# Optimization experiments

Hardware: AMD Instinct MI355X
Metric: run time of the kernel (lower is better)

Reference implementation:

```python
import jax, jax.numpy as jnp
import numpy as np

P_SCALAR = 40.0
NEG_INF = -1e9


def setup_inputs() -> dict:
    key = jax.random.key(0)
    ks = jax.random.split(key, 6)
    B, Dk, Dv, T, H, W = 2, 128, 512, 2, 64, 64
    qkey = jax.random.normal(ks[0], (B, Dk, H, W), dtype=jnp.float32)
    qval = jax.random.normal(ks[1], (B, Dv, H, W), dtype=jnp.float32)
    mkey = jax.random.normal(ks[2], (B, Dk, T, H, W), dtype=jnp.float32)
    mval = jax.random.normal(ks[3], (B, Dv, T, H, W), dtype=jnp.float32)
    qmask = jax.random.bernoulli(ks[4], 0.5, (B, 1, H, W))
    mmask = jax.random.bernoulli(ks[5], 0.5, (B, 1, T, H, W))
    return {"qkey": qkey, "qval": qval, "qmask": qmask,
            "mkey": mkey, "mval": mval, "mmask": mmask}


def reference(qkey, qval, qmask, mkey, mval, mmask):
    # Faithful vectorized version of maskRead: for each batch, attention from
    # masked query pixels over masked memory pixels, scatter back into zeros.
    # Boolean-gather + softmax over gathered rows == full softmax with masked
    # logits set to -inf (rows outside mmask get zero probability).
    B, Dk, H, W = qkey.shape
    Dv = qval.shape[1]
    qk = qkey.reshape(B, Dk, H * W)            # [B, Dk, Nq]
    mk = mkey.reshape(B, Dk, -1)               # [B, Dk, Nm]
    mv = mval.reshape(B, Dv, -1)               # [B, Dv, Nm]
    qm = qmask.reshape(B, H * W)               # [B, Nq]
    mm = mmask.reshape(B, -1)                  # [B, Nm]

    # p[b, m, q] = <mk[b,:,m], qk[b,:,q]> * p_scalar, softmax over m
    p = jnp.einsum('bdm,bdq->bmq', mk, qk) * P_SCALAR
    p = jnp.where(mm[:, :, None], p, NEG_INF)
    p = jax.nn.softmax(p, axis=1)              # [B, Nm, Nq]

    read = jnp.einsum('bvm,bmq->bvq', mv, p)   # [B, Dv, Nq]

    # zero out query pixels outside qmask; skip batches with empty masks
    valid = qm[:, None, :] & mm.any(axis=1)[:, None, None] & qm.any(axis=1)[:, None, None]
    qread = jnp.where(valid, read, 0.0)
    return qread.reshape(B, Dv, H, W)
```

## Files before the change

### kernel.cpp

```cpp
#include <hip/hip_runtime.h>

#define NQ 4096
#define NM 8192
#define DK 128
#define DV 512
#define BATCH 2
#define NT (NM / 64)
#define KTS 8192
#define VTILE 16384

typedef __attribute__((ext_vector_type(8))) short short8;
typedef __attribute__((ext_vector_type(4))) float f32x4;
typedef unsigned short ushort_t;

#define MF(A_, B_, C_) __builtin_amdgcn_mfma_f32_16x16x32_bf16(A_, B_, C_, 0, 0, 0)

static __device__ __forceinline__ unsigned short f2bf(float x) {
    union { float f; unsigned int u; } c; c.f = x;
    unsigned int u = c.u;
    return (unsigned short)((u + 0x7FFFu + ((u >> 16) & 1u)) >> 16);
}
static __device__ __forceinline__ float bf2f(unsigned short h) {
    union { unsigned int u; float f; } c; c.u = ((unsigned int)h) << 16;
    return c.f;
}

static __device__ __forceinline__ size_t vaddr(int b, int pos, int dv) {
    const int mt = pos >> 6, m64 = pos & 63;
    const int dvh = dv >> 8, rr = dv & 255;
    return (((size_t)(b * NT + mt) * 2 + dvh) * VTILE)
         + (rr >> 6) * 4096 + ((rr >> 4) & 3) * 1024
         + (m64 >> 5) * 512
         + ((((m64 >> 4) & 1) * 2 + ((m64 >> 3) & 1)) * 128)
         + (rr & 15) * 8 + (m64 & 7);
}

#define LOADK(AH, AL, itn_) do {                                              \
    const size_t ktb_ = kbase + (size_t)(itn_) * KTS;                         \
    _Pragma("unroll")                                                         \
    for (int ks_ = 0; ks_ < 4; ++ks_) {                                       \
        AH[ks_] = *(const short8*)(kh0 + ktb_ + ks_ * 512);                   \
        AL[ks_] = *(const short8*)(kl0 + ktb_ + ks_ * 512);                   \
    }                                                                         \
} while (0)

__global__ __launch_bounds__(1024) void scan_kernel(
    const int* __restrict__ qmask, const int* __restrict__ mmask,
    int* __restrict__ cidx, int* __restrict__ cpos,
    int* __restrict__ cnts, int* __restrict__ qflags) {
    const int b = blockIdx.x;
    const int t = threadIdx.x;
    const int lane = t & 63;
    const int w = t >> 6;
    __shared__ int wsum[16];
    __shared__ int qsh;

    const int* mp = mmask + b * NM;
    const int base = t * 8;
    int val[8];
#pragma unroll
    for (int i = 0; i < 8; ++i) val[i] = (mp[base + i] != 0);
    int c0 = 0;
#pragma unroll
    for (int i = 0; i < 8; ++i) c0 += val[i];

    int c = c0;
#pragma unroll
    for (int off = 1; off < 64; off <<= 1) {
        int n = __shfl_up(c, off, 64);
        if (lane >= off) c += n;
    }
    if (lane == 63) wsum[w] = c;
    if (t == 0) qsh = 0;
    __syncthreads();
    if (t == 0) {
        int s = 0;
#pragma unroll
        for (int i = 0; i < 16; ++i) { s += wsum[i]; wsum[i] = s; }
    }
    __syncthreads();
    const int wbase = (w == 0) ? 0 : wsum[w - 1];
    int run = wbase + (c - c0);
#pragma unroll
    for (int i = 0; i < 8; ++i) {
        int m = base + i;
        cpos[b * NM + m] = run;
        if (val[i]) { cidx[b * NM + run] = m; ++run; }
    }

    int qa = 0;
    for (int i = t; i < NQ; i += 1024) qa |= (qmask[b * NQ + i] != 0);
    if (qa) atomicOr(&qsh, 1);
    __syncthreads();
    if (t == 0) { cnts[b] = wsum[15]; qflags[b] = qsh; }
}

__global__ __launch_bounds__(256) void prep_q_kernel(
    const float* __restrict__ src, ushort_t* __restrict__ hi,
    ushort_t* __restrict__ lo) {
    const int b = blockIdx.z;
    const int d0 = blockIdx.y * 32;
    const int n0 = blockIdx.x * 32;
    __shared__ float t32[32][33];
    for (int l = threadIdx.x; l < 1024; l += 256) {
        int r = l >> 5, c = l & 31;
        t32[r][c] = src[((size_t)b * DK + d0 + r) * NQ + n0 + c];
    }
    __syncthreads();
    for (int l = threadIdx.x; l < 1024; l += 256) {
        int r = l >> 5, c = l & 31;
        float f = t32[c][r];
        unsigned short h = f2bf(f);
        unsigned short lw = f2bf(f - bf2f(h));
        size_t off = ((size_t)b * NQ + n0 + r) * DK + d0 + c;
        hi[off] = h;
        lo[off] = lw;
    }
}

__global__ __launch_bounds__(256) void prep_k_kernel(
    const float* __restrict__ src, const int* __restrict__ mmask,
    const int* __restrict__ cpos,
    ushort_t* __restrict__ hi, ushort_t* __restrict__ lo) {
    const int b = blockIdx.z;
    const int d0 = blockIdx.y * 32;
    const int n0 = blockIdx.x * 32;
    __shared__ float t32[32][33];
    for (int l = threadIdx.x; l < 1024; l += 256) {
        int r = l >> 5, c = l & 31;
        t32[r][c] = src[((size_t)b * DK + d0 + r) * NM + n0 + c];
    }
    __syncthreads();
    for (int l = threadIdx.x; l < 1024; l += 256) {
        int r = l >> 5, c = l & 31;
        int m = n0 + r;
        if (mmask[b * NM + m] != 0) {
            int pos = cpos[b * NM + m];
            float f = t32[c][r];
            unsigned short h = f2bf(f);
            unsigned short lw = f2bf(f - bf2f(h));
            int d = d0 + c;
            size_t off = ((size_t)(b * NT + (pos >> 6))) * KTS
                       + ((pos >> 4) & 3) * 2048 + (d >> 5) * 512
                       + ((d >> 3) & 3) * 128 + (pos & 15) * 8 + (d & 7);
            hi[off] = h;
            lo[off] = lw;
        }
    }
}

__global__ __launch_bounds__(256) void prep_v_kernel(
    const float* __restrict__ src, const int* __restrict__ mmask,
    const int* __restrict__ cpos, const int* __restrict__ cnts,
    ushort_t* __restrict__ dst) {
    const int b = blockIdx.z;
    const int dv0 = blockIdx.x * 8;
    if (blockIdx.y == 8) {
        const int cnt = cnts[b];
        const int pend = ((cnt + 63) >> 6) * 64;
        const int dv = dv0 + (threadIdx.x >> 5);
        for (int p = cnt + (threadIdx.x & 31); p < pend; p += 32)
            dst[vaddr(b, p, dv)] = 0;
        return;
    }
    const int m = blockIdx.y * 1024 + threadIdx.x * 4;
    const int4 mm = *(const int4*)(mmask + b * NM + m);
    const int4 cp = *(const int4*)(cpos + b * NM + m);
#pragma unroll
    for (int i = 0; i < 8; ++i) {
        const int dv = dv0 + i;
        const float4 v = *(const float4*)(src + ((size_t)b * DV + dv) * NM + m);
        if (mm.x) dst[vaddr(b, cp.x, dv)] = f2bf(v.x);
        if (mm.y) dst[vaddr(b, cp.y, dv)] = f2bf(v.y);
        if (mm.z) dst[vaddr(b, cp.z, dv)] = f2bf(v.z);
        if (mm.w) dst[vaddr(b, cp.w, dv)] = f2bf(v.w);
    }
}

__global__ __launch_bounds__(256, 4) void stats_kernel(
    const ushort_t* __restrict__ Qhi, const ushort_t* __restrict__ Khi,
    const int* __restrict__ cnts, float* __restrict__ mpart) {
    const int t = threadIdx.x;
    const int lane = t & 63;
    const int w = t >> 6;
    const int quad = lane >> 4;
    const int col = lane & 15;
    const int bid = blockIdx.x;
    const int part = bid & 3;
    const int b = (bid >> 2) & 1;
    const int qb = (bid >> 3) * 32;

    const int cnt = cnts[b];
    const int nit = (cnt + 63) >> 6;
    const int it0 = (nit * part) >> 2;
    const int it1 = (nit * (part + 1)) >> 2;

    __shared__ float red_m[4][32];

    short8 qfh[2][4];
    {
        const ushort_t* qhp = Qhi + ((size_t)b * NQ + qb) * DK;
#pragma unroll
        for (int qt = 0; qt < 2; ++qt)
#pragma unroll
            for (int ks = 0; ks < 4; ++ks)
                qfh[qt][ks] = *(const short8*)(qhp + (size_t)(qt * 16 + col) * DK + ks * 32 + quad * 8);
    }

    const f32x4 zero4 = {0.f, 0.f, 0.f, 0.f};
    float mloc[2] = {-3.0e38f, -3.0e38f};
    const ushort_t* kh0 = Khi + w * 2048 + lane * 8;
    const size_t kbase = (size_t)(b * NT) * KTS;

#define LOADKH(A_, itn_) do {                                                 \
    const size_t ktb_ = kbase + (size_t)(itn_) * KTS;                         \
    _Pragma("unroll")                                                         \
    for (int ks_ = 0; ks_ < 4; ++ks_)                                         \
        A_[ks_] = *(const short8*)(kh0 + ktb_ + ks_ * 512);                   \
} while (0)

#define STPH(CK, NK, it_, itn_) do {                                          \
    LOADKH(NK, itn_);                                                         \
    f32x4 aS0 = zero4, aS1 = zero4;                                           \
    _Pragma("unroll")                                                         \
    for (int ks = 0; ks < 4; ++ks) {                                          \
        aS0 = MF(CK[ks], qfh[0][ks], aS0);                                    \
        aS1 = MF(CK[ks], qfh[1][ks], aS1);                                    \
    }                                                                         \
    const int mrow_ = (it_) * 64 + w * 16 + quad * 4;                         \
    _Pragma("unroll")                                                         \
    for (int r = 0; r < 4; ++r) {                                             \
        if (mrow_ + r < cnt) {                                                \
            mloc[0] = fmaxf(mloc[0], aS0[r] * 40.0f);                         \
            mloc[1] = fmaxf(mloc[1], aS1[r] * 40.0f);                         \
        }                                                                     \
    }                                                                         \
} while (0)

    short8 kA[4], kB[4];
    int it = it0;
    if (it < it1) {
        LOADKH(kA, it);
        int itn;
        while (true) {
            itn = (it + 1 < it1) ? it + 1 : it;
            STPH(kA, kB, it, itn);
            if (++it >= it1) break;
            itn = (it + 1 < it1) ? it + 1 : it;
            STPH(kB, kA, it, itn);
            if (++it >= it1) break;
        }
    }
#undef STPH
#undef LOADKH

#pragma unroll
    for (int qt = 0; qt < 2; ++qt) {
        float m = mloc[qt];
        m = fmaxf(m, __shfl_xor(m, 16, 64));
        m = fmaxf(m, __shfl_xor(m, 32, 64));
        if (lane < 16) red_m[w][qt * 16 + col] = m;
    }
    __syncthreads();
    if (t < 32) {
        float M = -3.0e38f;
#pragma unroll
        for (int ww = 0; ww < 4; ++ww) M = fmaxf(M, red_m[ww][t]);
        mpart[((size_t)(b * 4 + part)) * NQ + qb + t] = M;
    }
}

__global__ __launch_bounds__(256, 2) void pv_kernel(
    const ushort_t* __restrict__ Qhi, const ushort_t* __restrict__ Qlo,
    const ushort_t* __restrict__ Khi, const ushort_t* __restrict__ Klo,
    const ushort_t* __restrict__ Vimg, const int* __restrict__ cnts,
    const float* __restrict__ mpart, float* __restrict__ out0,
    float* __restrict__ out1, float* __restrict__ lsum) {
    const int t = threadIdx.x;
    const int lane = t & 63;
    const int w = t >> 6;
    const int quad = lane >> 4;
    const int col = lane & 15;
    const int bid = blockIdx.x;
    const int chunk = bid & 1;
    const int dvh = (bid >> 1) & 1;
    const int b = (bid >> 2) & 1;
    const int qb = (bid >> 3) * 64;

    const int cnt = cnts[b];
    const int nit = (cnt + 63) >> 6;
    const int nh = (nit + 1) >> 1;
    const int it0 = chunk ? nh : 0;
    const int it1 = chunk ? nit : nh;

    __shared__ __align__(16) ushort_t Q_s[2][4][4][512];
    __shared__ __align__(16) ushort_t P_s[2][64][68];

    float gm[4];
#pragma unroll
    for (int qt = 0; qt < 4; ++qt) {
        float M = -3.0e38f;
#pragma unroll
        for (int c = 0; c < 4; ++c)
            M = fmaxf(M, mpart[((size_t)(b * 4 + c)) * NQ + qb + qt * 16 + col]);
        gm[qt] = M + 8.0f;
    }

    {
        const int r = t >> 2, ks4 = t & 3;
        const int qt_ = r >> 4, col_ = r & 15;
        const ushort_t* qhp = Qhi + ((size_t)b * NQ + qb + r) * DK + ks4 * 32;
        const ushort_t* qlp = Qlo + ((size_t)b * NQ + qb + r) * DK + ks4 * 32;
#pragma unroll
        for (int qd = 0; qd < 4; ++qd) {
            *(short8*)&Q_s[0][qt_][ks4][qd * 128 + col_ * 8] = *(const short8*)(qhp + qd * 8);
            *(short8*)&Q_s[1][qt_][ks4][qd * 128 + col_ * 8] = *(const short8*)(qlp + qd * 8);
        }
    }
    __syncthreads();

    const ushort_t* kh0 = Khi + w * 2048 + lane * 8;
    const ushort_t* kl0 = Klo + w * 2048 + lane * 8;
    const size_t kbase = (size_t)(b * NT) * KTS;
    const ushort_t* vl0 = Vimg + ((size_t)(b * NT) * 2 + dvh) * VTILE
                        + w * 4096 + lane * 8;

    const f32x4 zero4 = {0.f, 0.f, 0.f, 0.f};
    const short8 vones = {(short)0x3F80, (short)0x3F80, (short)0x3F80,
                          (short)0x3F80, (short)0x3F80, (short)0x3F80,
                          (short)0x3F80, (short)0x3F80};
    const bool doL = (dvh == 0) && (w == 0);
    f32x4 accO[4][4];
#pragma unroll
    for (int vt = 0; vt < 4; ++vt)
#pragma unroll
        for (int qt = 0; qt < 4; ++qt) accO[vt][qt] = zero4;
    f32x4 accL[4];
#pragma unroll
    for (int qt = 0; qt < 4; ++qt) accL[qt] = zero4;

    for (int it = it0; it < it1; ++it) {
        const int pb = (it - it0) & 1;
        short8 kh[4], kl[4];
        LOADK(kh, kl, it);
        f32x4 aS[4];
#pragma unroll
        for (int qt = 0; qt < 4; ++qt) aS[qt] = zero4;
#pragma unroll
        for (int qt = 0; qt < 4; ++qt) {
#pragma unroll
            for (int ks = 0; ks < 4; ++ks) {
                const short8 qh = *(const short8*)&Q_s[0][qt][ks][lane * 8];
                const short8 ql = *(const short8*)&Q_s[1][qt][ks][lane * 8];
                aS[qt] = MF(kh[ks], qh, aS[qt]);
                aS[qt] = MF(kh[ks], ql, aS[qt]);
                aS[qt] = MF(kl[ks], qh, aS[qt]);
            }
        }
        const ushort_t* vp = vl0 + (size_t)it * (2 * VTILE);
        short8 vf[4][2];
#pragma unroll
        for (int vt = 0; vt < 4; ++vt) {
            vf[vt][0] = *(const short8*)(vp + vt * 1024);
            vf[vt][1] = *(const short8*)(vp + vt * 1024 + 512);
        }
        const int mrow = it * 64 + w * 16 + quad * 4;
#pragma unroll
        for (int qt = 0; qt < 4; ++qt) {
            float p[4];
#pragma unroll
            for (int r = 0; r < 4; ++r)
                p[r] = (mrow + r < cnt) ? __expf(aS[qt][r] * 40.0f - gm[qt]) : 0.0f;
            ushort4 pk;
            pk.x = f2bf(p[0]); pk.y = f2bf(p[1]);
            pk.z = f2bf(p[2]); pk.w = f2bf(p[3]);
            *(ushort4*)&P_s[pb][qt * 16 + col][w * 16 + quad * 4] = pk;
        }
        asm volatile("s_waitcnt lgkmcnt(0)" ::: "memory");
        __builtin_amdgcn_s_barrier();
        __builtin_amdgcn_sched_barrier(0);
#pragma unroll
        for (int k2 = 0; k2 < 2; ++k2) {
            short8 pq[4];
#pragma unroll
            for (int qt = 0; qt < 4; ++qt)
                pq[qt] = *(const short8*)&P_s[pb][qt * 16 + col][k2 * 32 + quad * 8];
#pragma unroll
            for (int vt = 0; vt < 4; ++vt)
#pragma unroll
                for (int qt = 0; qt < 4; ++qt)
                    accO[vt][qt] = MF(vf[vt][k2], pq[qt], accO[vt][qt]);
            if (doL) {
#pragma unroll
                for (int qt = 0; qt < 4; ++qt)
                    accL[qt] = MF(vones, pq[qt], accL[qt]);
            }
        }
    }

    float* pbase = chunk ? out1 : out0;
#pragma unroll
    for (int qt = 0; qt < 4; ++qt) {
        const int q = qb + qt * 16 + col;
#pragma unroll
        for (int vt = 0; vt < 4; ++vt)
#pragma unroll
            for (int r = 0; r < 4; ++r) {
                int dv = dvh * 256 + w * 64 + vt * 16 + quad * 4 + r;
                pbase[((size_t)b * DV + dv) * NQ + q] = accO[vt][qt][r];
            }
    }
    if (doL && lane < 16) {
#pragma unroll
        for (int qt = 0; qt < 4; ++qt)
            lsum[((size_t)(b * 2 + chunk)) * NQ + qb + qt * 16 + col] = accL[qt][0];
    }
}

__global__ __launch_bounds__(256) void combine_kernel(
    const float* p0, const float* __restrict__ p1,
    const float* __restrict__ lsum, const int* __restrict__ cnts,
    const int* __restrict__ qflags, const int* __restrict__ qmask,
    float* out) {
    const size_t i = ((size_t)blockIdx.x * 256 + threadIdx.x) * 4;
    const int b = (int)(i >> 21);
    const int q = (int)(i & (NQ - 1));
    f32x4 a = *(const f32x4*)(p0 + i);
    f32x4 c = *(const f32x4*)(p1 + i);
    f32x4 l0 = *(const f32x4*)(lsum + (size_t)(b * 2) * NQ + q);
    f32x4 l1 = *(const f32x4*)(lsum + (size_t)(b * 2 + 1) * NQ + q);
    const int4 qm = *(const int4*)(qmask + b * NQ + q);
    const bool bv = (qflags[b] != 0) && (cnts[b] > 0);
    f32x4 r;
    float lv;
    lv = l0[0] + l1[0]; r[0] = (bv && qm.x && lv > 0.f) ? (a[0] + c[0]) / lv : 0.f;
    lv = l0[1] + l1[1]; r[1] = (bv && qm.y && lv > 0.f) ? (a[1] + c[1]) / lv : 0.f;
    lv = l0[2] + l1[2]; r[2] = (bv && qm.z && lv > 0.f) ? (a[2] + c[2]) / lv : 0.f;
    lv = l0[3] + l1[3]; r[3] = (bv && qm.w && lv > 0.f) ? (a[3] + c[3]) / lv : 0.f;
    *(f32x4*)(out + i) = r;
}

extern "C" void kernel_launch(void* const* d_in, const int* in_sizes, int n_in,
                              void* d_out, int out_size, void* d_ws, size_t ws_size,
                              hipStream_t stream) {
    const float* qkey  = (const float*)d_in[0];
    const int*   qmask = (const int*)d_in[2];
    const float* mkey  = (const float*)d_in[3];
    const float* mval  = (const float*)d_in[4];
    const int*   mmask = (const int*)d_in[5];
    float* out = (float*)d_out;

    char* ws = (char*)d_ws;
    size_t off = 0;
    const size_t QS  = (size_t)BATCH * NQ * DK * 2;
    const size_t KS2 = (size_t)BATCH * NM * DK * 2;
    const size_t VS  = (size_t)BATCH * NT * 2 * VTILE * 2;
    const size_t OS  = (size_t)BATCH * DV * NQ * 4;
    ushort_t* Qhi = (ushort_t*)(ws + off); off += QS;
    ushort_t* Qlo = (ushort_t*)(ws + off); off += QS;
    ushort_t* Khi = (ushort_t*)(ws + off); off += KS2;
    ushort_t* Klo = (ushort_t*)(ws + off); off += KS2;
    ushort_t* Vc  = (ushort_t*)(ws + off); off += VS;
    float* part1  = (float*)(ws + off); off += OS;
    float* mpart  = (float*)(ws + off); off += (size_t)BATCH * 4 * NQ * 4;
    float* lsum   = (float*)(ws + off); off += (size_t)BATCH * 2 * NQ * 4;
    int* cidx     = (int*)(ws + off); off += (size_t)BATCH * NM * 4;
    int* cpos     = (int*)(ws + off); off += (size_t)BATCH * NM * 4;
    int* cnts     = (int*)(ws + off); off += 64;
    int* qflags   = (int*)(ws + off); off += 64;

    scan_kernel<<<BATCH, 1024, 0, stream>>>(qmask, mmask, cidx, cpos, cnts, qflags);

    dim3 gq(NQ / 32, DK / 32, BATCH);
    prep_q_kernel<<<gq, 256, 0, stream>>>(qkey, Qhi, Qlo);
    dim3 gk(NM / 32, DK / 32, BATCH);
    prep_k_kernel<<<gk, 256, 0, stream>>>(mkey, mmask, cpos, Khi, Klo);

    dim3 gv(DV / 8, 9, BATCH);
    prep_v_kernel<<<gv, 256, 0, stream>>>(mval, mmask, cpos, cnts, Vc);

    stats_kernel<<<(NQ / 32) * 8, 256, 0, stream>>>(Qhi, Khi, cnts, mpart);

    pv_kernel<<<(NQ / 64) * 8, 256, 0, stream>>>(
        Qhi, Qlo, Khi, Klo, Vc, cnts, mpart, out, part1, lsum);

    combine_kernel<<<(int)((size_t)BATCH * DV * NQ / 1024), 256, 0, stream>>>(
        out, part1, lsum, cnts, qflags, qmask, out);
}
```

Before: 237.4 us.

## Merge prep kernels, widen stats query tile, split PV into three key chunks

The three prep kernels (Q, K, V conversion) are merged into one launch that dispatches on block index. The stats kernel now covers 64 queries per block instead of 32, so each K fragment load is reused across four query tiles. The PV kernel splits the key range into three chunks instead of two, which raises the block count to 768, and its occupancy hint goes to 3. This needs a third partial output buffer and lsum slot, and the combine kernel now reads more data.

```diff
diff --git a/kernel.cpp b/kernel.cpp
--- a/kernel.cpp
+++ b/kernel.cpp
@@ -95,89 +95,90 @@
     if (t == 0) { cnts[b] = wsum[15]; qflags[b] = qsh; }
 }
 
-__global__ __launch_bounds__(256) void prep_q_kernel(
-    const float* __restrict__ src, ushort_t* __restrict__ hi,
-    ushort_t* __restrict__ lo) {
-    const int b = blockIdx.z;
-    const int d0 = blockIdx.y * 32;
-    const int n0 = blockIdx.x * 32;
+__global__ __launch_bounds__(256) void prep_all_kernel(
+    const float* __restrict__ qkey, const float* __restrict__ mkey,
+    const float* __restrict__ mval, const int* __restrict__ mmask,
+    const int* __restrict__ cpos, const int* __restrict__ cnts,
+    ushort_t* __restrict__ Qhi, ushort_t* __restrict__ Qlo,
+    ushort_t* __restrict__ Khi, ushort_t* __restrict__ Klo,
+    ushort_t* __restrict__ Vc) {
     __shared__ float t32[32][33];
-    for (int l = threadIdx.x; l < 1024; l += 256) {
-        int r = l >> 5, c = l & 31;
-        t32[r][c] = src[((size_t)b * DK + d0 + r) * NQ + n0 + c];
-    }
-    __syncthreads();
-    for (int l = threadIdx.x; l < 1024; l += 256) {
-        int r = l >> 5, c = l & 31;
-        float f = t32[c][r];
-        unsigned short h = f2bf(f);
-        unsigned short lw = f2bf(f - bf2f(h));
-        size_t off = ((size_t)b * NQ + n0 + r) * DK + d0 + c;
-        hi[off] = h;
-        lo[off] = lw;
-    }
-}
-
-__global__ __launch_bounds__(256) void prep_k_kernel(
-    const float* __restrict__ src, const int* __restrict__ mmask,
-    const int* __restrict__ cpos,
-    ushort_t* __restrict__ hi, ushort_t* __restrict__ lo) {
-    const int b = blockIdx.z;
-    const int d0 = blockIdx.y * 32;
-    const int n0 = blockIdx.x * 32;
-    __shared__ float t32[32][33];
-    for (int l = threadIdx.x; l < 1024; l += 256) {
-        int r = l >> 5, c = l & 31;
-        t32[r][c] = src[((size_t)b * DK + d0 + r) * NM + n0 + c];
-    }
-    __syncthreads();
-    for (int l = threadIdx.x; l < 1024; l += 256) {
-        int r = l >> 5, c = l & 31;
-        int m = n0 + r;
-        if (mmask[b * NM + m] != 0) {
-            int pos = cpos[b * NM + m];
+    const int g = blockIdx.x;
+
+    if (g < 1024) {
+        const int bx = g & 127, by = (g >> 7) & 3, b = g >> 9;
+        const int d0 = by * 32, n0 = bx * 32;
+        for (int l = threadIdx.x; l < 1024; l += 256) {
+            int r = l >> 5, c = l & 31;
+            t32[r][c] = qkey[((size_t)b * DK + d0 + r) * NQ + n0 + c];
+        }
+        __syncthreads();
+        for (int l = threadIdx.x; l < 1024; l += 256) {
+            int r = l >> 5, c = l & 31;
             float f = t32[c][r];
             unsigned short h = f2bf(f);
             unsigned short lw = f2bf(f - bf2f(h));
-            int d = d0 + c;
-            size_t off = ((size_t)(b * NT + (pos >> 6))) * KTS
-                       + ((pos >> 4) & 3) * 2048 + (d >> 5) * 512
-                       + ((d >> 3) & 3) * 128 + (pos & 15) * 8 + (d & 7);
-            hi[off] = h;
-            lo[off] = lw;
-        }
-    }
-}
-
-__global__ __launch_bounds__(256) void prep_v_kernel(
-    const float* __restrict__ src, const int* __restrict__ mmask,
-    const int* __restrict__ cpos, const int* __restrict__ cnts,
-    ushort_t* __restrict__ dst) {
-    const int b = blockIdx.z;
-    const int dv0 = blockIdx.x * 8;
-    if (blockIdx.y == 8) {
+            size_t off = ((size_t)b * NQ + n0 + r) * DK + d0 + c;
+            Qhi[off] = h;
+            Qlo[off] = lw;
+        }
+        return;
+    }
+    if (g < 3072) {
+        const int h0 = g - 1024;
+        const int bx = h0 & 255, by = (h0 >> 8) & 3, b = h0 >> 10;
+        const int d0 = by * 32, n0 = bx * 32;
+        for (int l = threadIdx.x; l < 1024; l += 256) {
+            int r = l >> 5, c = l & 31;
+            t32[r][c] = mkey[((size_t)b * DK + d0 + r) * NM + n0 + c];
+        }
+        __syncthreads();
+        for (int l = threadIdx.x; l < 1024; l += 256) {
+            int r = l >> 5, c = l & 31;
+            int m = n0 + r;
+            if (mmask[b * NM + m] != 0) {
+                int pos = cpos[b * NM + m];
+                float f = t32[c][r];
+                unsigned short hh = f2bf(f);
+                unsigned short lw = f2bf(f - bf2f(hh));
+                int d = d0 + c;
+                size_t off = ((size_t)(b * NT + (pos >> 6))) * KTS
+                           + ((pos >> 4) & 3) * 2048 + (d >> 5) * 512
+                           + ((d >> 3) & 3) * 128 + (pos & 15) * 8 + (d & 7);
+                Khi[off] = hh;
+                Klo[off] = lw;
+            }
+        }
+        return;
+    }
+    const int h0 = g - 3072;
+    const int bx = h0 & 63;
+    const int by = (h0 >> 6) % 9;
+    const int b = h0 / 576;
+    const int dv0 = bx * 8;
+    if (by == 8) {
         const int cnt = cnts[b];
         const int pend = ((cnt + 63) >> 6) * 64;
         const int dv = dv0 + (threadIdx.x >> 5);
         for (int p = cnt + (threadIdx.x & 31); p < pend; p += 32)
-            dst[vaddr(b, p, dv)] = 0;
+            Vc[vaddr(b, p, dv)] = 0;
         return;
     }
-    const int m = blockIdx.y * 1024 + threadIdx.x * 4;
+    const int m = by * 1024 + threadIdx.x * 4;
     const int4 mm = *(const int4*)(mmask + b * NM + m);
     const int4 cp = *(const int4*)(cpos + b * NM + m);
 #pragma unroll
     for (int i = 0; i < 8; ++i) {
         const int dv = dv0 + i;
-        const float4 v = *(const float4*)(src + ((size_t)b * DV + dv) * NM + m);
-        if (mm.x) dst[vaddr(b, cp.x, dv)] = f2bf(v.x);
-        if (mm.y) dst[vaddr(b, cp.y, dv)] = f2bf(v.y);
-        if (mm.z) dst[vaddr(b, cp.z, dv)] = f2bf(v.z);
-        if (mm.w) dst[vaddr(b, cp.w, dv)] = f2bf(v.w);
-    }
-}
-
-__global__ __launch_bounds__(256, 4) void stats_kernel(
+        const float4 v = *(const float4*)(mval + ((size_t)b * DV + dv) * NM + m);
+        if (mm.x) Vc[vaddr(b, cp.x, dv)] = f2bf(v.x);
+        if (mm.y) Vc[vaddr(b, cp.y, dv)] = f2bf(v.y);
+        if (mm.z) Vc[vaddr(b, cp.z, dv)] = f2bf(v.z);
+        if (mm.w) Vc[vaddr(b, cp.w, dv)] = f2bf(v.w);
+    }
+}
+
+__global__ __launch_bounds__(256, 3) void stats_kernel(
     const ushort_t* __restrict__ Qhi, const ushort_t* __restrict__ Khi,
     const int* __restrict__ cnts, float* __restrict__ mpart) {
     const int t = threadIdx.x;
@@ -188,27 +189,27 @@
     const int bid = blockIdx.x;
     const int part = bid & 3;
     const int b = (bid >> 2) & 1;
-    const int qb = (bid >> 3) * 32;
+    const int qb = (bid >> 3) * 64;
 
     const int cnt = cnts[b];
     const int nit = (cnt + 63) >> 6;
     const int it0 = (nit * part) >> 2;
     const int it1 = (nit * (part + 1)) >> 2;
 
-    __shared__ float red_m[4][32];
-
-    short8 qfh[2][4];
+    __shared__ float red_m[4][64];
+
+    short8 qfh[4][4];
     {
         const ushort_t* qhp = Qhi + ((size_t)b * NQ + qb) * DK;
 #pragma unroll
-        for (int qt = 0; qt < 2; ++qt)
+        for (int qt = 0; qt < 4; ++qt)
 #pragma unroll
             for (int ks = 0; ks < 4; ++ks)
                 qfh[qt][ks] = *(const short8*)(qhp + (size_t)(qt * 16 + col) * DK + ks * 32 + quad * 8);
     }
 
     const f32x4 zero4 = {0.f, 0.f, 0.f, 0.f};
-    float mloc[2] = {-3.0e38f, -3.0e38f};
+    float mloc[4] = {-3.0e38f, -3.0e38f, -3.0e38f, -3.0e38f};
     const ushort_t* kh0 = Khi + w * 2048 + lane * 8;
     const size_t kbase = (size_t)(b * NT) * KTS;
 
@@ -221,18 +222,21 @@
 
 #define STPH(CK, NK, it_, itn_) do {                                          \
     LOADKH(NK, itn_);                                                         \
-    f32x4 aS0 = zero4, aS1 = zero4;                                           \
+    f32x4 aS[4];                                                              \
     _Pragma("unroll")                                                         \
-    for (int ks = 0; ks < 4; ++ks) {                                          \
-        aS0 = MF(CK[ks], qfh[0][ks], aS0);                                    \
-        aS1 = MF(CK[ks], qfh[1][ks], aS1);                                    \
-    }                                                                         \
+    for (int qt = 0; qt < 4; ++qt) aS[qt] = zero4;                            \
+    _Pragma("unroll")                                                         \
+    for (int ks = 0; ks < 4; ++ks)                                            \
+        _Pragma("unroll")                                                     \
+        for (int qt = 0; qt < 4; ++qt)                                        \
+            aS[qt] = MF(CK[ks], qfh[qt][ks], aS[qt]);                         \
     const int mrow_ = (it_) * 64 + w * 16 + quad * 4;                         \
     _Pragma("unroll")                                                         \
     for (int r = 0; r < 4; ++r) {                                             \
         if (mrow_ + r < cnt) {                                                \
-            mloc[0] = fmaxf(mloc[0], aS0[r] * 40.0f);                         \
-            mloc[1] = fmaxf(mloc[1], aS1[r] * 40.0f);                         \
+            _Pragma("unroll")                                                 \
+            for (int qt = 0; qt < 4; ++qt)                                    \
+                mloc[qt] = fmaxf(mloc[qt], aS[qt][r] * 40.0f);                \
         }                                                                     \
     }                                                                         \
 } while (0)
@@ -255,14 +259,14 @@
 #undef LOADKH
 
 #pragma unroll
-    for (int qt = 0; qt < 2; ++qt) {
+    for (int qt = 0; qt < 4; ++qt) {
         float m = mloc[qt];
         m = fmaxf(m, __shfl_xor(m, 16, 64));
         m = fmaxf(m, __shfl_xor(m, 32, 64));
         if (lane < 16) red_m[w][qt * 16 + col] = m;
     }
     __syncthreads();
-    if (t < 32) {
+    if (t < 64) {
         float M = -3.0e38f;
 #pragma unroll
         for (int ww = 0; ww < 4; ++ww) M = fmaxf(M, red_m[ww][t]);
@@ -270,28 +274,29 @@
     }
 }
 
-__global__ __launch_bounds__(256, 2) void pv_kernel(
+__global__ __launch_bounds__(256, 3) void pv_kernel(
     const ushort_t* __restrict__ Qhi, const ushort_t* __restrict__ Qlo,
     const ushort_t* __restrict__ Khi, const ushort_t* __restrict__ Klo,
     const ushort_t* __restrict__ Vimg, const int* __restrict__ cnts,
     const float* __restrict__ mpart, float* __restrict__ out0,
-    float* __restrict__ out1, float* __restrict__ lsum) {
+    float* __restrict__ out1, float* __restrict__ out2,
+    float* __restrict__ lsum) {
     const int t = threadIdx.x;
     const int lane = t & 63;
     const int w = t >> 6;
     const int quad = lane >> 4;
     const int col = lane & 15;
     const int bid = blockIdx.x;
-    const int chunk = bid & 1;
+    const int b = bid & 1;
     const int dvh = (bid >> 1) & 1;
-    const int b = (bid >> 2) & 1;
-    const int qb = (bid >> 3) * 64;
+    const int r3 = bid >> 2;
+    const int chunk = r3 % 3;
+    const int qb = (r3 / 3) * 64;
 
     const int cnt = cnts[b];
     const int nit = (cnt + 63) >> 6;
-    const int nh = (nit + 1) >> 1;
-    const int it0 = chunk ? nh : 0;
-    const int it1 = chunk ? nit : nh;
+    const int it0 = (nit * chunk) / 3;
+    const int it1 = (nit * (chunk + 1)) / 3;
 
     __shared__ __align__(16) ushort_t Q_s[2][4][4][512];
     __shared__ __align__(16) ushort_t P_s[2][64][68];
@@ -398,7 +403,7 @@
         }
     }
 
-    float* pbase = chunk ? out1 : out0;
+    float* pbase = (chunk == 0) ? out0 : ((chunk == 1) ? out1 : out2);
 #pragma unroll
     for (int qt = 0; qt < 4; ++qt) {
         const int q = qb + qt * 16 + col;
@@ -413,30 +418,32 @@
     if (doL && lane < 16) {
 #pragma unroll
         for (int qt = 0; qt < 4; ++qt)
-            lsum[((size_t)(b * 2 + chunk)) * NQ + qb + qt * 16 + col] = accL[qt][0];
+            lsum[((size_t)(b * 3 + chunk)) * NQ + qb + qt * 16 + col] = accL[qt][0];
     }
 }
 
 __global__ __launch_bounds__(256) void combine_kernel(
     const float* p0, const float* __restrict__ p1,
-    const float* __restrict__ lsum, const int* __restrict__ cnts,
-    const int* __restrict__ qflags, const int* __restrict__ qmask,
-    float* out) {
+    const float* __restrict__ p2, const float* __restrict__ lsum,
+    const int* __restrict__ cnts, const int* __restrict__ qflags,
+    const int* __restrict__ qmask, float* out) {
     const size_t i = ((size_t)blockIdx.x * 256 + threadIdx.x) * 4;
     const int b = (int)(i >> 21);
     const int q = (int)(i & (NQ - 1));
     f32x4 a = *(const f32x4*)(p0 + i);
     f32x4 c = *(const f32x4*)(p1 + i);
-    f32x4 l0 = *(const f32x4*)(lsum + (size_t)(b * 2) * NQ + q);
-    f32x4 l1 = *(const f32x4*)(lsum + (size_t)(b * 2 + 1) * NQ + q);
+    f32x4 d = *(const f32x4*)(p2 + i);
+    f32x4 l0 = *(const f32x4*)(lsum + (size_t)(b * 3) * NQ + q);
+    f32x4 l1 = *(const f32x4*)(lsum + (size_t)(b * 3 + 1) * NQ + q);
+    f32x4 l2 = *(const f32x4*)(lsum + (size_t)(b * 3 + 2) * NQ + q);
     const int4 qm = *(const int4*)(qmask + b * NQ + q);
     const bool bv = (qflags[b] != 0) && (cnts[b] > 0);
     f32x4 r;
     float lv;
-    lv = l0[0] + l1[0]; r[0] = (bv && qm.x && lv > 0.f) ? (a[0] + c[0]) / lv : 0.f;
-    lv = l0[1] + l1[1]; r[1] = (bv && qm.y && lv > 0.f) ? (a[1] + c[1]) / lv : 0.f;
-    lv = l0[2] + l1[2]; r[2] = (bv && qm.z && lv > 0.f) ? (a[2] + c[2]) / lv : 0.f;
-    lv = l0[3] + l1[3]; r[3] = (bv && qm.w && lv > 0.f) ? (a[3] + c[3]) / lv : 0.f;
+    lv = l0[0] + l1[0] + l2[0]; r[0] = (bv && qm.x && lv > 0.f) ? (a[0] + c[0] + d[0]) / lv : 0.f;
+    lv = l0[1] + l1[1] + l2[1]; r[1] = (bv && qm.y && lv > 0.f) ? (a[1] + c[1] + d[1]) / lv : 0.f;
+    lv = l0[2] + l1[2] + l2[2]; r[2] = (bv && qm.z && lv > 0.f) ? (a[2] + c[2] + d[2]) / lv : 0.f;
+    lv = l0[3] + l1[3] + l2[3]; r[3] = (bv && qm.w && lv > 0.f) ? (a[3] + c[3] + d[3]) / lv : 0.f;
     *(f32x4*)(out + i) = r;
 }
 
@@ -462,8 +469,9 @@
     ushort_t* Klo = (ushort_t*)(ws + off); off += KS2;
     ushort_t* Vc  = (ushort_t*)(ws + off); off += VS;
     float* part1  = (float*)(ws + off); off += OS;
+    float* part2  = (float*)(ws + off); off += OS;
     float* mpart  = (float*)(ws + off); off += (size_t)BATCH * 4 * NQ * 4;
-    float* lsum   = (float*)(ws + off); off += (size_t)BATCH * 2 * NQ * 4;
+    float* lsum   = (float*)(ws + off); off += (size_t)BATCH * 3 * NQ * 4;
     int* cidx     = (int*)(ws + off); off += (size_t)BATCH * NM * 4;
     int* cpos     = (int*)(ws + off); off += (size_t)BATCH * NM * 4;
     int* cnts     = (int*)(ws + off); off += 64;
@@ -471,19 +479,14 @@
 
     scan_kernel<<<BATCH, 1024, 0, stream>>>(qmask, mmask, cidx, cpos, cnts, qflags);
 
-    dim3 gq(NQ / 32, DK / 32, BATCH);
-    prep_q_kernel<<<gq, 256, 0, stream>>>(qkey, Qhi, Qlo);
-    dim3 gk(NM / 32, DK / 32, BATCH);
-    prep_k_kernel<<<gk, 256, 0, stream>>>(mkey, mmask, cpos, Khi, Klo);
-
-    dim3 gv(DV / 8, 9, BATCH);
-    prep_v_kernel<<<gv, 256, 0, stream>>>(mval, mmask, cpos, cnts, Vc);
-
-    stats_kernel<<<(NQ / 32) * 8, 256, 0, stream>>>(Qhi, Khi, cnts, mpart);
-
-    pv_kernel<<<(NQ / 64) * 8, 256, 0, stream>>>(
-        Qhi, Qlo, Khi, Klo, Vc, cnts, mpart, out, part1, lsum);
+    prep_all_kernel<<<4224, 256, 0, stream>>>(
+        qkey, mkey, mval, mmask, cpos, cnts, Qhi, Qlo, Khi, Klo, Vc);
+
+    stats_kernel<<<(NQ / 64) * 8, 256, 0, stream>>>(Qhi, Khi, cnts, mpart);
+
+    pv_kernel<<<(NQ / 64) * 12, 256, 0, stream>>>(
+        Qhi, Qlo, Khi, Klo, Vc, cnts, mpart, out, part1, part2, lsum);
 
     combine_kernel<<<(int)((size_t)BATCH * DV * NQ / 1024), 256, 0, stream>>>(
-        out, part1, lsum, cnts, qflags, qmask, out);
-}
+        out, part1, part2, lsum, cnts, qflags, qmask, out);
+}
```

Result: no change. 233.9 us (-1.5%).
